# Kernel tuning notes

Hardware: AMD Instinct MI355X
Metric: run time of the kernel (lower is better)

The kernel has to match this reference:

```python
import jax, jax.numpy as jnp
import numpy as np

N = 50000
E = 800000
NDIM_IN = 128
NDIM_OUT = 64
H = 3
EDIM = 8
CLASS_NUM = 10
NEG_SLOPE = 0.2  # DGL GATConv default negative_slope


def _gat_layer(src, dst, x, W, a_l, a_r, b):
    """One DGL-style GATConv layer. x: [N, Fin]; W: [Fin, H*D]; a_l/a_r: [H, D]; b: [H*D]."""
    n, hd = x.shape[0], W.shape[1]
    D = hd // H
    f = (x @ W).reshape(n, H, D)                         # projected feats [N,H,D]
    el = (f * a_l[None]).sum(-1)                          # [N,H]
    er = (f * a_r[None]).sum(-1)                          # [N,H]
    e = jax.nn.leaky_relu(el[src] + er[dst], NEG_SLOPE)   # [E,H] per-edge logits
    m = jax.ops.segment_max(e, dst, num_segments=n)       # softmax max per dst node
    ex = jnp.exp(e - m[dst])                              # [E,H]
    denom = jax.ops.segment_sum(ex, dst, num_segments=n)  # [N,H]
    alpha = ex / denom[dst]                               # edge softmax
    out = jax.ops.segment_sum(f[src] * alpha[:, :, None], dst, num_segments=n)  # [N,H,D]
    return out + b.reshape(1, H, D)


def setup_inputs() -> dict:
    key = jax.random.key(0)
    ks = jax.random.split(key, 16)
    src = jax.random.randint(ks[0], (E,), 0, N)
    dst = jax.random.randint(ks[1], (E,), 0, N)
    nfeats = jax.random.normal(ks[2], (N, NDIM_IN), dtype=jnp.float32)
    efeats = jax.random.normal(ks[3], (E, EDIM), dtype=jnp.float32)
    s1 = 1.0 / np.sqrt(NDIM_IN)
    s2 = 1.0 / np.sqrt(H * NDIM_OUT)
    sp = 1.0 / np.sqrt(2 * H * NDIM_OUT)
    W1 = jax.random.normal(ks[4], (NDIM_IN, H * NDIM_OUT), dtype=jnp.float32) * s1
    al1 = jax.random.normal(ks[5], (H, NDIM_OUT), dtype=jnp.float32) * s1
    ar1 = jax.random.normal(ks[6], (H, NDIM_OUT), dtype=jnp.float32) * s1
    b1 = jnp.zeros((H * NDIM_OUT,), dtype=jnp.float32)
    W2 = jax.random.normal(ks[7], (H * NDIM_OUT, H * NDIM_OUT), dtype=jnp.float32) * s2
    al2 = jax.random.normal(ks[8], (H, NDIM_OUT), dtype=jnp.float32) * s2
    ar2 = jax.random.normal(ks[9], (H, NDIM_OUT), dtype=jnp.float32) * s2
    b2 = jnp.zeros((H * NDIM_OUT,), dtype=jnp.float32)
    Wp = jax.random.normal(ks[10], (2 * H * NDIM_OUT, CLASS_NUM), dtype=jnp.float32) * sp
    bp = jnp.zeros((CLASS_NUM,), dtype=jnp.float32)
    return {"src": src, "dst": dst, "nfeats": nfeats, "efeats": efeats,
            "W1": W1, "al1": al1, "ar1": ar1, "b1": b1,
            "W2": W2, "al2": al2, "ar2": ar2, "b2": b2,
            "Wp": Wp, "bp": bp}


def reference(src, dst, nfeats, efeats, W1, al1, ar1, b1, W2, al2, ar2, b2, Wp, bp):
    # efeats is accepted but unused, matching the original forward signature.
    h = _gat_layer(src, dst, nfeats, W1, al1, ar1, b1)      # [N,H,D]
    h = jax.nn.relu(h.reshape(h.shape[0], -1))              # [N,H*D]
    h = _gat_layer(src, dst, h, W2, al2, ar2, b2)           # [N,H,D]
    h = jax.nn.relu(h.reshape(h.shape[0], -1))              # [N,H*D]
    # MLPPredictor: per-edge concat(src,dst) -> linear
    score = jnp.concatenate([h[src], h[dst]], axis=1) @ Wp + bp  # [E,class_num]
    return score
```

## Files before the change

kernel.cpp:

```cpp
#include <hip/hip_runtime.h>
#include <cstdint>

constexpr int KIN = 128;
constexpr int HD  = 192;
constexpr int NC  = 10;
#define NEG_SLOPE 0.2f

typedef __attribute__((ext_vector_type(8))) short bf16x8;
typedef __attribute__((ext_vector_type(4))) float f32x4;

__device__ __forceinline__ float b2f(unsigned short u) {
    union { unsigned int i; float f; } x; x.i = ((unsigned int)u) << 16; return x.f;
}
__device__ __forceinline__ unsigned short f2b(float f) {
    union { float f; unsigned int i; } x; x.f = f;
    unsigned int r = x.i + 0x7FFFu + ((x.i >> 16) & 1u);
    return (unsigned short)(r >> 16);
}
__device__ __forceinline__ float gload(const void* p, long i, int isbf) {
    return isbf ? b2f(((const unsigned short*)p)[i]) : ((const float*)p)[i];
}
__device__ __forceinline__ float lrelu(float v) { return v > 0.f ? v : NEG_SLOPE * v; }

__global__ void k_prep(const void* __restrict__ nfeats, const void* __restrict__ W1,
                       const void* __restrict__ W2, const void* __restrict__ Wp,
                       unsigned short* __restrict__ xb, int* __restrict__ deg,
                       unsigned short* __restrict__ Bp1, unsigned short* __restrict__ Bp2,
                       unsigned short* __restrict__ BpPQ, int N, long nx,
                       int bZ, int bC, int* __restrict__ flag) {
    __shared__ int shIsb;
    if (threadIdx.x == 0) {
        const unsigned short* u = (const unsigned short*)W1;
        float mx = 0.f;
        for (int i = 0; i < 64; ++i) {
            float v = fabsf(b2f(u[i]));
            if (!(v < 1e30f)) v = 1e30f;
            mx = fmaxf(mx, v);
        }
        shIsb = (mx < 1e4f) ? 1 : 0;
        if (blockIdx.x == 0) *flag = shIsb;
    }
    __syncthreads();
    int isb = shIsb;
    int b = blockIdx.x, tid = threadIdx.x;
    if (b < bZ) { int i = b * 256 + tid; if (i < N) deg[i] = 0; return; }
    b -= bZ;
    if (b < bC) { long i = (long)b * 256 + tid; if (i < nx) xb[i] = f2b(gload(nfeats, i, isb)); return; }
    b -= bC;
    int t = b * 256 + tid;
    const int s1 = 12 * 4 * 512, s2 = s1 + 12 * 6 * 512, s3 = s2 + 6 * 512, s4 = s3 + 6 * 512;
    const void* W; unsigned short* Bp; int K, Creal, CT, KS; long rowOff; int tt;
    if (t < s1)      { W = W1; Bp = Bp1;            K = KIN; Creal = HD; CT = 12; KS = 4; rowOff = 0;  tt = t; }
    else if (t < s2) { W = W2; Bp = Bp2;            K = HD;  Creal = HD; CT = 12; KS = 6; rowOff = 0;  tt = t - s1; }
    else if (t < s3) { W = Wp; Bp = BpPQ;           K = HD;  Creal = NC; CT = 1;  KS = 6; rowOff = 0;  tt = t - s2; }
    else if (t < s4) { W = Wp; Bp = BpPQ + 6 * 512; K = HD;  Creal = NC; CT = 1;  KS = 6; rowOff = HD; tt = t - s3; }
    else return;
    int j = tt & 7, lane = (tt >> 3) & 63, ks = (tt >> 9) % KS, ct = tt / (KS * 512);
    int k = ks * 32 + ((lane >> 4) << 3) + j;
    int c = ct * 16 + (lane & 15);
    float v = 0.f;
    if (k < K && c < Creal) v = gload(W, (rowOff + k) * (long)Creal + c, isb);
    Bp[tt] = f2b(v);
}

template<int CT, int KS, int ELR>
__global__ void k_mm(const unsigned short* __restrict__ A, const unsigned short* __restrict__ Bp,
                     unsigned short* __restrict__ fb, const void* __restrict__ al,
                     const void* __restrict__ ar, float* __restrict__ el4,
                     float* __restrict__ er4, int M, int Cout, const int* __restrict__ flag) {
    int wid = threadIdx.x >> 6, lane = threadIdx.x & 63;
    int rt = blockIdx.x * 4 + wid;
    if (rt * 16 >= M) return;
    const int K = KS * 32;
    int mrow = rt * 16 + (lane & 15);
    int kq = (lane >> 4) << 3;
    f32x4 acc[CT];
#pragma unroll
    for (int ct = 0; ct < CT; ++ct) acc[ct] = (f32x4){0.f, 0.f, 0.f, 0.f};
    const unsigned short* arow = A + (long)mrow * K + kq;
    const bf16x8* bp = (const bf16x8*)Bp;
#pragma unroll
    for (int ks = 0; ks < KS; ++ks) {
        bf16x8 a = *(const bf16x8*)(arow + ks * 32);
#pragma unroll
        for (int ct = 0; ct < CT; ++ct) {
            bf16x8 b = bp[(ct * KS + ks) * 64 + lane];
            acc[ct] = __builtin_amdgcn_mfma_f32_16x16x32_bf16(a, b, acc[ct], 0, 0, 0);
        }
    }
    int quad = lane >> 4, c0 = lane & 15;
    int rbase = rt * 16 + quad * 4;
#pragma unroll
    for (int ct = 0; ct < CT; ++ct)
#pragma unroll
        for (int r = 0; r < 4; ++r)
            fb[(long)(rbase + r) * Cout + ct * 16 + c0] = f2b(acc[ct][r]);
    if (ELR) {
        int isb = *flag;
        float pl[3][4], pr[3][4];
#pragma unroll
        for (int h = 0; h < 3; ++h)
#pragma unroll
            for (int r = 0; r < 4; ++r) { pl[h][r] = 0.f; pr[h][r] = 0.f; }
#pragma unroll
        for (int ct = 0; ct < CT; ++ct) {
            int h = ct >> 2;
            float wl = gload(al, ct * 16 + c0, isb);
            float wr = gload(ar, ct * 16 + c0, isb);
#pragma unroll
            for (int r = 0; r < 4; ++r) {
                pl[h][r] += acc[ct][r] * wl;
                pr[h][r] += acc[ct][r] * wr;
            }
        }
#pragma unroll
        for (int d = 1; d < 16; d <<= 1)
#pragma unroll
            for (int h = 0; h < 3; ++h)
#pragma unroll
                for (int r = 0; r < 4; ++r) {
                    pl[h][r] += __shfl_xor(pl[h][r], d);
                    pr[h][r] += __shfl_xor(pr[h][r], d);
                }
        if (c0 == 0) {
#pragma unroll
            for (int r = 0; r < 4; ++r)
#pragma unroll
                for (int h = 0; h < 3; ++h) {
                    el4[(long)(rbase + r) * 4 + h] = pl[h][r];
                    er4[(long)(rbase + r) * 4 + h] = pr[h][r];
                }
        }
    }
}

__global__ void k_mmpq(const unsigned short* __restrict__ A, const unsigned short* __restrict__ Bp,
                       float* __restrict__ PQ, int M) {
    constexpr int CT = 2, KS = 6;
    int wid = threadIdx.x >> 6, lane = threadIdx.x & 63;
    int rt = blockIdx.x * 4 + wid;
    if (rt * 16 >= M) return;
    const int K = KS * 32;
    int mrow = rt * 16 + (lane & 15);
    int kq = (lane >> 4) << 3;
    f32x4 acc[CT];
#pragma unroll
    for (int ct = 0; ct < CT; ++ct) acc[ct] = (f32x4){0.f, 0.f, 0.f, 0.f};
    const unsigned short* arow = A + (long)mrow * K + kq;
    const bf16x8* bp = (const bf16x8*)Bp;
#pragma unroll
    for (int ks = 0; ks < KS; ++ks) {
        bf16x8 a = *(const bf16x8*)(arow + ks * 32);
#pragma unroll
        for (int ct = 0; ct < CT; ++ct) {
            bf16x8 b = bp[(ct * KS + ks) * 64 + lane];
            acc[ct] = __builtin_amdgcn_mfma_f32_16x16x32_bf16(a, b, acc[ct], 0, 0, 0);
        }
    }
    int quad = lane >> 4, c0 = lane & 15;
    int rbase = rt * 16 + quad * 4;
    if (c0 < NC) {
#pragma unroll
        for (int ct = 0; ct < CT; ++ct)
#pragma unroll
            for (int r = 0; r < 4; ++r)
                PQ[(long)(rbase + r) * (2 * NC) + ct * NC + c0] = acc[ct][r];
    }
}

__global__ void k_hist(const int* __restrict__ dst, int E, int* __restrict__ deg) {
    int i = blockIdx.x * blockDim.x + threadIdx.x;
    if (i < E) atomicAdd(&deg[dst[i]], 1);
}

__global__ void k_scan1(const int* __restrict__ deg, int n, int* __restrict__ off,
                        int* __restrict__ bsum) {
    __shared__ int sh[1024];
    int tid = threadIdx.x, i = blockIdx.x * 1024 + tid;
    int v = (i < n) ? deg[i] : 0;
    sh[tid] = v;
    __syncthreads();
    for (int s = 1; s < 1024; s <<= 1) {
        int t = (tid >= s) ? sh[tid - s] : 0;
        __syncthreads();
        sh[tid] += t;
        __syncthreads();
    }
    if (i < n) off[i] = sh[tid] - v;
    if (tid == 1023) bsum[blockIdx.x] = sh[tid];
}

__global__ void k_scan2(int* __restrict__ bsum, int nb, int* __restrict__ off, int n) {
    int tid = threadIdx.x;
    int v = (tid < nb) ? bsum[tid] : 0;
    int incl = v;
    for (int s = 1; s < 64; s <<= 1) {
        int t = __shfl_up(incl, s);
        if (tid >= s) incl += t;
    }
    if (tid < nb) bsum[tid] = incl - v;
    if (tid == 63) off[n] = incl;
}

__global__ void k_scan3(int* __restrict__ off, const int* __restrict__ bsum, int n,
                        int* __restrict__ cur) {
    int i = blockIdx.x * 1024 + threadIdx.x;
    if (i < n) {
        int v = off[i] + bsum[blockIdx.x];
        off[i] = v;
        cur[i] = v;
    }
}

__global__ void k_fill(const int* __restrict__ src, const int* __restrict__ dst, int E,
                       int* __restrict__ cur, int* __restrict__ csr) {
    int i = blockIdx.x * blockDim.x + threadIdx.x;
    if (i < E) {
        int p = atomicAdd(&cur[dst[i]], 1);
        csr[p] = src[i];
    }
}

__global__ void __launch_bounds__(256, 8)
k_agg(const unsigned int* __restrict__ fbu, const float4* __restrict__ el4,
      const float* __restrict__ er4, const int* __restrict__ off,
      const int* __restrict__ csr, const void* __restrict__ bias,
      unsigned int* __restrict__ outu, int Nn, const int* __restrict__ flag) {
    int lane = threadIdx.x & 63;
    int n = blockIdx.x * 4 + (threadIdx.x >> 6);
    if (n >= Nn) return;
    int isb = *flag;
    int s0 = off[n], s1 = off[n + 1];
    int deg = s1 - s0;
    float er0 = er4[n * 4 + 0], er1 = er4[n * 4 + 1], er2 = er4[n * 4 + 2];
    bool lo32 = lane < 32;
    float aa0 = 0.f, aa1 = 0.f, ab0 = 0.f, ab1 = 0.f;

    if (deg > 0 && deg <= 64) {
        int e = s0 + lane;
        bool on = e < s1;
        int sIdx = on ? csr[e] : 0;
        float4 el = el4[sIdx];
        float t0 = on ? lrelu(el.x + er0) : -1e30f;
        float t1 = on ? lrelu(el.y + er1) : -1e30f;
        float t2 = on ? lrelu(el.z + er2) : -1e30f;
        float m0 = t0, m1 = t1, m2 = t2;
        for (int d = 1; d < 64; d <<= 1) {
            m0 = fmaxf(m0, __shfl_xor(m0, d));
            m1 = fmaxf(m1, __shfl_xor(m1, d));
            m2 = fmaxf(m2, __shfl_xor(m2, d));
        }
        float w0 = on ? __expf(t0 - m0) : 0.f;
        float w1 = on ? __expf(t1 - m1) : 0.f;
        float w2 = on ? __expf(t2 - m2) : 0.f;
        float d0 = w0, d1 = w1, d2 = w2;
        for (int d = 1; d < 64; d <<= 1) {
            d0 += __shfl_xor(d0, d);
            d1 += __shfl_xor(d1, d);
            d2 += __shfl_xor(d2, d);
        }
        w0 *= 1.f / d0; w1 *= 1.f / d1; w2 *= 1.f / d2;
#pragma unroll 8
        for (int j = 0; j < deg; ++j) {
            int s = __shfl(sIdx, j);
            float u0 = __shfl(w0, j), u1 = __shfl(w1, j), u2 = __shfl(w2, j);
            float wa = lo32 ? u0 : u1;
            const unsigned int* fr = fbu + (long)s * 96;
            unsigned int ua = fr[lane];
            aa0 += wa * b2f((unsigned short)ua);
            aa1 += wa * b2f((unsigned short)(ua >> 16));
            if (lo32) {
                unsigned int ub = fr[64 + lane];
                ab0 += u2 * b2f((unsigned short)ub);
                ab1 += u2 * b2f((unsigned short)(ub >> 16));
            }
        }
    } else if (deg > 64) {
        float m0 = -1e30f, m1 = -1e30f, m2 = -1e30f;
        for (int e = s0 + lane; e < s1; e += 64) {
            float4 el = el4[csr[e]];
            m0 = fmaxf(m0, lrelu(el.x + er0));
            m1 = fmaxf(m1, lrelu(el.y + er1));
            m2 = fmaxf(m2, lrelu(el.z + er2));
        }
        for (int d = 1; d < 64; d <<= 1) {
            m0 = fmaxf(m0, __shfl_xor(m0, d));
            m1 = fmaxf(m1, __shfl_xor(m1, d));
            m2 = fmaxf(m2, __shfl_xor(m2, d));
        }
        float d0 = 0.f, d1 = 0.f, d2 = 0.f;
        for (int e = s0 + lane; e < s1; e += 64) {
            float4 el = el4[csr[e]];
            d0 += __expf(lrelu(el.x + er0) - m0);
            d1 += __expf(lrelu(el.y + er1) - m1);
            d2 += __expf(lrelu(el.z + er2) - m2);
        }
        for (int d = 1; d < 64; d <<= 1) {
            d0 += __shfl_xor(d0, d);
            d1 += __shfl_xor(d1, d);
            d2 += __shfl_xor(d2, d);
        }
        float id0 = 1.f / d0, id1 = 1.f / d1, id2 = 1.f / d2;
        for (int e = s0; e < s1; ++e) {
            int s = csr[e];
            float4 el = el4[s];
            float u0 = __expf(lrelu(el.x + er0) - m0) * id0;
            float u1 = __expf(lrelu(el.y + er1) - m1) * id1;
            float u2 = __expf(lrelu(el.z + er2) - m2) * id2;
            float wa = lo32 ? u0 : u1;
            const unsigned int* fr = fbu + (long)s * 96;
            unsigned int ua = fr[lane];
            aa0 += wa * b2f((unsigned short)ua);
            aa1 += wa * b2f((unsigned short)(ua >> 16));
            if (lo32) {
                unsigned int ub = fr[64 + lane];
                ab0 += u2 * b2f((unsigned short)ub);
                ab1 += u2 * b2f((unsigned short)(ub >> 16));
            }
        }
    }
    int ca = 2 * lane;
    aa0 = fmaxf(aa0 + gload(bias, ca,     isb), 0.f);
    aa1 = fmaxf(aa1 + gload(bias, ca + 1, isb), 0.f);
    unsigned int* orow = outu + (long)n * 96;
    orow[lane] = (unsigned)f2b(aa0) | ((unsigned)f2b(aa1) << 16);
    if (lo32) {
        int cb = 128 + 2 * lane;
        ab0 = fmaxf(ab0 + gload(bias, cb,     isb), 0.f);
        ab1 = fmaxf(ab1 + gload(bias, cb + 1, isb), 0.f);
        orow[64 + lane] = (unsigned)f2b(ab0) | ((unsigned)f2b(ab1) << 16);
    }
}

__global__ void k_score(const int* __restrict__ src, const int* __restrict__ dst,
                        const float* __restrict__ PQ, const void* __restrict__ bp,
                        void* __restrict__ out, int E, const int* __restrict__ flag) {
    __shared__ float sh[256 * NC];
    int tid = threadIdx.x;
    int e0 = blockIdx.x * 256;
    int e = e0 + tid;
    int isb = *flag;
    float v[NC];
    if (e < E) {
        const float* pr = PQ + (long)src[e] * (2 * NC);
        const float* qr = PQ + (long)dst[e] * (2 * NC) + NC;
#pragma unroll
        for (int c = 0; c < NC; ++c) v[c] = pr[c] + qr[c] + gload(bp, c, isb);
    }
    int nE = min(256, E - e0);
    if (isb) {
        unsigned int* shu = (unsigned int*)sh;
        if (e < E) {
#pragma unroll
            for (int c = 0; c < NC / 2; ++c)
                shu[tid * (NC / 2) + c] =
                    (unsigned)f2b(v[2 * c]) | ((unsigned)f2b(v[2 * c + 1]) << 16);
        }
        __syncthreads();
        int nU = nE * (NC / 2);
        unsigned int* ob = (unsigned int*)((unsigned short*)out + (long)e0 * NC);
        int nU4 = nU >> 2;
        uint4* ob4 = (uint4*)ob;
        const uint4* sb4 = (const uint4*)shu;
        for (int u = tid; u < nU4; u += 256) ob4[u] = sb4[u];
        for (int w = (nU4 << 2) + tid; w < nU; w += 256) ob[w] = shu[w];
    } else {
        if (e < E) {
#pragma unroll
            for (int c = 0; c < NC; ++c) sh[tid * NC + c] = v[c];
        }
        __syncthreads();
        int nU = nE * NC;
        float* ob = (float*)out + (long)e0 * NC;
        int nU4 = nU >> 2;
        float4* ob4 = (float4*)ob;
        const float4* sb4 = (const float4*)sh;
        for (int u = tid; u < nU4; u += 256) ob4[u] = sb4[u];
        for (int w = (nU4 << 2) + tid; w < nU; w += 256) ob[w] = sh[w];
    }
}

extern "C" void kernel_launch(void* const* d_in, const int* in_sizes, int n_in,
                              void* d_out, int out_size, void* d_ws, size_t ws_size,
                              hipStream_t stream) {
    const int* src = (const int*)d_in[0];
    const int* dst = (const int*)d_in[1];
    const void* nfeats = d_in[2];
    const void* W1  = d_in[4];
    const void* al1 = d_in[5];
    const void* ar1 = d_in[6];
    const void* b1  = d_in[7];
    const void* W2  = d_in[8];
    const void* al2 = d_in[9];
    const void* ar2 = d_in[10];
    const void* b2  = d_in[11];
    const void* Wp  = d_in[12];
    const void* bp  = d_in[13];

    const int E = in_sizes[0];
    const int N = in_sizes[2] / KIN;

    size_t o = 0;
    auto alloc = [&](size_t bytes) { size_t r = o; o = (o + bytes + 255) & ~(size_t)255; return r; };
    char* ws = (char*)d_ws;
    int*   flag = (int*)  (ws + alloc(4));
    int*   deg  = (int*)  (ws + alloc((size_t)N * 4));
    int*   off  = (int*)  (ws + alloc((size_t)(N + 1) * 4));
    int*   cur  = (int*)  (ws + alloc((size_t)N * 4));
    int*   bsum = (int*)  (ws + alloc(64 * 4));
    int*   csr  = (int*)  (ws + alloc((size_t)E * 4));
    unsigned short* xb  = (unsigned short*)(ws + alloc((size_t)N * KIN * 2));
    unsigned short* fb  = (unsigned short*)(ws + alloc((size_t)N * HD * 2));
    unsigned short* hb  = (unsigned short*)(ws + alloc((size_t)N * HD * 2));
    unsigned short* Bp1 = (unsigned short*)(ws + alloc((size_t)12 * 4 * 512 * 2));
    unsigned short* Bp2 = (unsigned short*)(ws + alloc((size_t)12 * 6 * 512 * 2));
    unsigned short* BpPQ= (unsigned short*)(ws + alloc((size_t)2 * 6 * 512 * 2));
    float* el4  = (float*)(ws + alloc((size_t)N * 16));
    float* er4  = (float*)(ws + alloc((size_t)N * 16));
    float* PQ   = (float*)(ws + alloc((size_t)N * 2 * NC * 4));
    (void)ws_size; (void)n_in; (void)out_size;

    const int TB = 256;
    long nx = (long)N * KIN;
    int gE   = (E + TB - 1) / TB;
    int gAgg = (N + 3) / 4;
    int rowTiles = (N + 15) / 16;
    int gMM  = (rowTiles + 3) / 4;
    int nb   = (N + 1023) / 1024;

    int bZ = (N + TB - 1) / TB;
    int bC = (int)((nx + TB - 1) / TB);
    int bP = (12 * 4 * 512 + 12 * 6 * 512 + 2 * 6 * 512 + TB - 1) / TB;
    k_prep<<<bZ + bC + bP, TB, 0, stream>>>(nfeats, W1, W2, Wp, xb, deg,
                                            Bp1, Bp2, BpPQ, N, nx, bZ, bC, flag);

    k_hist<<<gE, TB, 0, stream>>>(dst, E, deg);
    k_scan1<<<nb, 1024, 0, stream>>>(deg, N, off, bsum);
    k_scan2<<<1, 64, 0, stream>>>(bsum, nb, off, N);
    k_scan3<<<nb, 1024, 0, stream>>>(off, bsum, N, cur);
    k_fill<<<gE, TB, 0, stream>>>(src, dst, E, cur, csr);

    k_mm<12, 4, 1><<<gMM, TB, 0, stream>>>(xb, Bp1, fb, al1, ar1, el4, er4, N, HD, flag);
    k_agg<<<gAgg, TB, 0, stream>>>((const unsigned int*)fb, (const float4*)el4, er4,
                                   off, csr, b1, (unsigned int*)hb, N, flag);

    k_mm<12, 6, 1><<<gMM, TB, 0, stream>>>(hb, Bp2, fb, al2, ar2, el4, er4, N, HD, flag);
    k_agg<<<gAgg, TB, 0, stream>>>((const unsigned int*)fb, (const float4*)el4, er4,
                                   off, csr, b2, (unsigned int*)hb, N, flag);

    k_mmpq<<<gMM, TB, 0, stream>>>(hb, BpPQ, PQ, N);
    k_score<<<gE, TB, 0, stream>>>(src, dst, PQ, bp, d_out, E, flag);
}
```

Measured before the change: 497.2 us.

## Restructure GAT aggregation with LDS edge weights and skip bf16 input conversion

The aggregation kernel now stores each edge's source index and softmax weights in shared memory. 48 lanes then each gather 4 contiguous bf16 features (uint2) per edge, with a 4-way unrolled loop. This replaces per-edge shuffles and the split 64+32 lane loads, aiming to raise memory-level parallelism and cut instruction overhead. Separately, when inputs are already bf16 the first matmul reads nfeats directly and the prep kernel skips the conversion copy. The __launch_bounds__ occupancy hint is dropped, and 16 lanes per wave now sit idle during gathers.

After: 441.3 us. 11.2% less time.

```diff
diff --git a/kernel.cpp b/kernel.cpp
--- a/kernel.cpp
+++ b/kernel.cpp
@@ -11,6 +11,12 @@
 
 __device__ __forceinline__ float b2f(unsigned short u) {
     union { unsigned int i; float f; } x; x.i = ((unsigned int)u) << 16; return x.f;
+}
+__device__ __forceinline__ float b2f_lo(unsigned int u) {
+    union { unsigned int i; float f; } x; x.i = u << 16; return x.f;
+}
+__device__ __forceinline__ float b2f_hi(unsigned int u) {
+    union { unsigned int i; float f; } x; x.i = u & 0xffff0000u; return x.f;
 }
 __device__ __forceinline__ unsigned short f2b(float f) {
     union { float f; unsigned int i; } x; x.f = f;
@@ -45,15 +51,20 @@
     int b = blockIdx.x, tid = threadIdx.x;
     if (b < bZ) { int i = b * 256 + tid; if (i < N) deg[i] = 0; return; }
     b -= bZ;
-    if (b < bC) { long i = (long)b * 256 + tid; if (i < nx) xb[i] = f2b(gload(nfeats, i, isb)); return; }
+    if (b < bC) {
+        if (isb) return;
+        long i = (long)b * 256 + tid;
+        if (i < nx) xb[i] = f2b(gload(nfeats, i, isb));
+        return;
+    }
     b -= bC;
     int t = b * 256 + tid;
     const int s1 = 12 * 4 * 512, s2 = s1 + 12 * 6 * 512, s3 = s2 + 6 * 512, s4 = s3 + 6 * 512;
-    const void* W; unsigned short* Bp; int K, Creal, CT, KS; long rowOff; int tt;
-    if (t < s1)      { W = W1; Bp = Bp1;            K = KIN; Creal = HD; CT = 12; KS = 4; rowOff = 0;  tt = t; }
-    else if (t < s2) { W = W2; Bp = Bp2;            K = HD;  Creal = HD; CT = 12; KS = 6; rowOff = 0;  tt = t - s1; }
-    else if (t < s3) { W = Wp; Bp = BpPQ;           K = HD;  Creal = NC; CT = 1;  KS = 6; rowOff = 0;  tt = t - s2; }
-    else if (t < s4) { W = Wp; Bp = BpPQ + 6 * 512; K = HD;  Creal = NC; CT = 1;  KS = 6; rowOff = HD; tt = t - s3; }
+    const void* W; unsigned short* Bp; int K, Creal, KS; long rowOff; int tt;
+    if (t < s1)      { W = W1; Bp = Bp1;            K = KIN; Creal = HD; KS = 4; rowOff = 0;  tt = t; }
+    else if (t < s2) { W = W2; Bp = Bp2;            K = HD;  Creal = HD; KS = 6; rowOff = 0;  tt = t - s1; }
+    else if (t < s3) { W = Wp; Bp = BpPQ;           K = HD;  Creal = NC; KS = 6; rowOff = 0;  tt = t - s2; }
+    else if (t < s4) { W = Wp; Bp = BpPQ + 6 * 512; K = HD;  Creal = NC; KS = 6; rowOff = HD; tt = t - s3; }
     else return;
     int j = tt & 7, lane = (tt >> 3) & 63, ks = (tt >> 9) % KS, ct = tt / (KS * 512);
     int k = ks * 32 + ((lane >> 4) << 3) + j;
@@ -64,13 +75,16 @@
 }
 
 template<int CT, int KS, int ELR>
-__global__ void k_mm(const unsigned short* __restrict__ A, const unsigned short* __restrict__ Bp,
+__global__ void k_mm(const void* __restrict__ Ain, const unsigned short* __restrict__ xbA,
+                     const unsigned short* __restrict__ Bp,
                      unsigned short* __restrict__ fb, const void* __restrict__ al,
                      const void* __restrict__ ar, float* __restrict__ el4,
                      float* __restrict__ er4, int M, int Cout, const int* __restrict__ flag) {
     int wid = threadIdx.x >> 6, lane = threadIdx.x & 63;
     int rt = blockIdx.x * 4 + wid;
     if (rt * 16 >= M) return;
+    int isb = *flag;
+    const unsigned short* A = isb ? (const unsigned short*)Ain : xbA;
     const int K = KS * 32;
     int mrow = rt * 16 + (lane & 15);
     int kq = (lane >> 4) << 3;
@@ -96,7 +110,6 @@
         for (int r = 0; r < 4; ++r)
             fb[(long)(rbase + r) * Cout + ct * 16 + c0] = f2b(acc[ct][r]);
     if (ELR) {
-        int isb = *flag;
         float pl[3][4], pr[3][4];
 #pragma unroll
         for (int h = 0; h < 3; ++h)
@@ -221,25 +234,25 @@
     }
 }
 
-__global__ void __launch_bounds__(256, 8)
-k_agg(const unsigned int* __restrict__ fbu, const float4* __restrict__ el4,
-      const float* __restrict__ er4, const int* __restrict__ off,
-      const int* __restrict__ csr, const void* __restrict__ bias,
-      unsigned int* __restrict__ outu, int Nn, const int* __restrict__ flag) {
+__global__ void k_agg(const unsigned int* __restrict__ fbu, const float4* __restrict__ el4,
+                      const float* __restrict__ er4, const int* __restrict__ off,
+                      const int* __restrict__ csr, const void* __restrict__ bias,
+                      unsigned int* __restrict__ outu, int Nn, const int* __restrict__ flag) {
+    __shared__ float4 shW[4][64];
     int lane = threadIdx.x & 63;
-    int n = blockIdx.x * 4 + (threadIdx.x >> 6);
+    int wv = threadIdx.x >> 6;
+    int n = blockIdx.x * 4 + wv;
     if (n >= Nn) return;
     int isb = *flag;
     int s0 = off[n], s1 = off[n + 1];
     int deg = s1 - s0;
     float er0 = er4[n * 4 + 0], er1 = er4[n * 4 + 1], er2 = er4[n * 4 + 2];
-    bool lo32 = lane < 32;
-    float aa0 = 0.f, aa1 = 0.f, ab0 = 0.f, ab1 = 0.f;
-
-    if (deg > 0 && deg <= 64) {
-        int e = s0 + lane;
-        bool on = e < s1;
-        int sIdx = on ? csr[e] : 0;
+    int hsel = lane >> 4;
+    float a0 = 0.f, a1 = 0.f, a2 = 0.f, a3 = 0.f;
+
+    if (deg <= 64) {
+        bool on = lane < deg;
+        int sIdx = on ? csr[s0 + lane] : 0;
         float4 el = el4[sIdx];
         float t0 = on ? lrelu(el.x + er0) : -1e30f;
         float t1 = on ? lrelu(el.y + er1) : -1e30f;
@@ -260,22 +273,39 @@
             d2 += __shfl_xor(d2, d);
         }
         w0 *= 1.f / d0; w1 *= 1.f / d1; w2 *= 1.f / d2;
-#pragma unroll 8
-        for (int j = 0; j < deg; ++j) {
-            int s = __shfl(sIdx, j);
-            float u0 = __shfl(w0, j), u1 = __shfl(w1, j), u2 = __shfl(w2, j);
-            float wa = lo32 ? u0 : u1;
-            const unsigned int* fr = fbu + (long)s * 96;
-            unsigned int ua = fr[lane];
-            aa0 += wa * b2f((unsigned short)ua);
-            aa1 += wa * b2f((unsigned short)(ua >> 16));
-            if (lo32) {
-                unsigned int ub = fr[64 + lane];
-                ab0 += u2 * b2f((unsigned short)ub);
-                ab1 += u2 * b2f((unsigned short)(ub >> 16));
+        shW[wv][lane] = make_float4(__int_as_float(sIdx), w0, w1, w2);
+        if (lane < 48) {
+            const float4* wr = shW[wv];
+            long lb = 2 * lane;
+            int j = 0;
+            for (; j + 4 <= deg; j += 4) {
+                float4 r0 = wr[j], r1 = wr[j + 1], r2 = wr[j + 2], r3 = wr[j + 3];
+                uint2 u0 = *(const uint2*)(fbu + (long)__float_as_int(r0.x) * 96 + lb);
+                uint2 u1 = *(const uint2*)(fbu + (long)__float_as_int(r1.x) * 96 + lb);
+                uint2 u2 = *(const uint2*)(fbu + (long)__float_as_int(r2.x) * 96 + lb);
+                uint2 u3 = *(const uint2*)(fbu + (long)__float_as_int(r3.x) * 96 + lb);
+                float q0 = hsel == 0 ? r0.y : (hsel == 1 ? r0.z : r0.w);
+                float q1 = hsel == 0 ? r1.y : (hsel == 1 ? r1.z : r1.w);
+                float q2 = hsel == 0 ? r2.y : (hsel == 1 ? r2.z : r2.w);
+                float q3 = hsel == 0 ? r3.y : (hsel == 1 ? r3.z : r3.w);
+                a0 += q0 * b2f_lo(u0.x); a1 += q0 * b2f_hi(u0.x);
+                a2 += q0 * b2f_lo(u0.y); a3 += q0 * b2f_hi(u0.y);
+                a0 += q1 * b2f_lo(u1.x); a1 += q1 * b2f_hi(u1.x);
+                a2 += q1 * b2f_lo(u1.y); a3 += q1 * b2f_hi(u1.y);
+                a0 += q2 * b2f_lo(u2.x); a1 += q2 * b2f_hi(u2.x);
+                a2 += q2 * b2f_lo(u2.y); a3 += q2 * b2f_hi(u2.y);
+                a0 += q3 * b2f_lo(u3.x); a1 += q3 * b2f_hi(u3.x);
+                a2 += q3 * b2f_lo(u3.y); a3 += q3 * b2f_hi(u3.y);
             }
-        }
-    } else if (deg > 64) {
+            for (; j < deg; ++j) {
+                float4 r0 = wr[j];
+                uint2 u0 = *(const uint2*)(fbu + (long)__float_as_int(r0.x) * 96 + lb);
+                float q0 = hsel == 0 ? r0.y : (hsel == 1 ? r0.z : r0.w);
+                a0 += q0 * b2f_lo(u0.x); a1 += q0 * b2f_hi(u0.x);
+                a2 += q0 * b2f_lo(u0.y); a3 += q0 * b2f_hi(u0.y);
+            }
+        }
+    } else {
         float m0 = -1e30f, m1 = -1e30f, m2 = -1e30f;
         for (int e = s0 + lane; e < s1; e += 64) {
             float4 el = el4[csr[e]];
@@ -300,35 +330,33 @@
             d1 += __shfl_xor(d1, d);
             d2 += __shfl_xor(d2, d);
         }
-        float id0 = 1.f / d0, id1 = 1.f / d1, id2 = 1.f / d2;
-        for (int e = s0; e < s1; ++e) {
-            int s = csr[e];
-            float4 el = el4[s];
-            float u0 = __expf(lrelu(el.x + er0) - m0) * id0;
-            float u1 = __expf(lrelu(el.y + er1) - m1) * id1;
-            float u2 = __expf(lrelu(el.z + er2) - m2) * id2;
-            float wa = lo32 ? u0 : u1;
-            const unsigned int* fr = fbu + (long)s * 96;
-            unsigned int ua = fr[lane];
-            aa0 += wa * b2f((unsigned short)ua);
-            aa1 += wa * b2f((unsigned short)(ua >> 16));
-            if (lo32) {
-                unsigned int ub = fr[64 + lane];
-                ab0 += u2 * b2f((unsigned short)ub);
-                ab1 += u2 * b2f((unsigned short)(ub >> 16));
+        if (lane < 48) {
+            float mh  = hsel == 0 ? m0 : (hsel == 1 ? m1 : m2);
+            float dh  = hsel == 0 ? d0 : (hsel == 1 ? d1 : d2);
+            float erh = hsel == 0 ? er0 : (hsel == 1 ? er1 : er2);
+            float idh = 1.f / dh;
+            long lb = 2 * lane;
+            for (int e = s0; e < s1; ++e) {
+                int s = csr[e];
+                float4 el = el4[s];
+                float eh = hsel == 0 ? el.x : (hsel == 1 ? el.y : el.z);
+                float w = __expf(lrelu(eh + erh) - mh) * idh;
+                uint2 u = *(const uint2*)(fbu + (long)s * 96 + lb);
+                a0 += w * b2f_lo(u.x); a1 += w * b2f_hi(u.x);
+                a2 += w * b2f_lo(u.y); a3 += w * b2f_hi(u.y);
             }
         }
     }
-    int ca = 2 * lane;
-    aa0 = fmaxf(aa0 + gload(bias, ca,     isb), 0.f);
-    aa1 = fmaxf(aa1 + gload(bias, ca + 1, isb), 0.f);
-    unsigned int* orow = outu + (long)n * 96;
-    orow[lane] = (unsigned)f2b(aa0) | ((unsigned)f2b(aa1) << 16);
-    if (lo32) {
-        int cb = 128 + 2 * lane;
-        ab0 = fmaxf(ab0 + gload(bias, cb,     isb), 0.f);
-        ab1 = fmaxf(ab1 + gload(bias, cb + 1, isb), 0.f);
-        orow[64 + lane] = (unsigned)f2b(ab0) | ((unsigned)f2b(ab1) << 16);
+    if (lane < 48) {
+        int c = 4 * lane;
+        a0 = fmaxf(a0 + gload(bias, c,     isb), 0.f);
+        a1 = fmaxf(a1 + gload(bias, c + 1, isb), 0.f);
+        a2 = fmaxf(a2 + gload(bias, c + 2, isb), 0.f);
+        a3 = fmaxf(a3 + gload(bias, c + 3, isb), 0.f);
+        uint2 o;
+        o.x = (unsigned)f2b(a0) | ((unsigned)f2b(a1) << 16);
+        o.y = (unsigned)f2b(a2) | ((unsigned)f2b(a3) << 16);
+        *(uint2*)(outu + (long)n * 96 + 2 * lane) = o;
     }
 }
 
@@ -440,11 +468,11 @@
     k_scan3<<<nb, 1024, 0, stream>>>(off, bsum, N, cur);
     k_fill<<<gE, TB, 0, stream>>>(src, dst, E, cur, csr);
 
-    k_mm<12, 4, 1><<<gMM, TB, 0, stream>>>(xb, Bp1, fb, al1, ar1, el4, er4, N, HD, flag);
+    k_mm<12, 4, 1><<<gMM, TB, 0, stream>>>(nfeats, xb, Bp1, fb, al1, ar1, el4, er4, N, HD, flag);
     k_agg<<<gAgg, TB, 0, stream>>>((const unsigned int*)fb, (const float4*)el4, er4,
                                    off, csr, b1, (unsigned int*)hb, N, flag);
 
-    k_mm<12, 6, 1><<<gMM, TB, 0, stream>>>(hb, Bp2, fb, al2, ar2, el4, er4, N, HD, flag);
+    k_mm<12, 6, 1><<<gMM, TB, 0, stream>>>(hb, hb, Bp2, fb, al2, ar2, el4, er4, N, HD, flag);
     k_agg<<<gAgg, TB, 0, stream>>>((const unsigned int*)fb, (const float4*)el4, er4,
                                    off, csr, b2, (unsigned int*)hb, N, flag);
 
```
